# Performance work log

Hardware: AMD Instinct MI355X
Metric: run time of the kernel (lower is better)

## Reference

```python
import jax, jax.numpy as jnp
import numpy as np
import math

N = 8192
NFEAT = 63
NHID = 1024
NLAYERS = 7
LAMBDA = 1.5
ALPHA = 0.7
NEG = -1e12


def setup_inputs() -> dict:
    key = jax.random.key(0)
    ks = jax.random.split(key, 12)
    x = jax.random.normal(ks[0], (N, NFEAT), dtype=jnp.float32)
    # dist acts as a (normalized) propagation matrix; scale by 1/N for numerical stability
    dist = jax.random.uniform(ks[1], (N, N), dtype=jnp.float32) / N
    adj = jax.random.randint(ks[2], (N, N), 0, 2, dtype=jnp.int32)
    # parameters
    fc_W = jax.random.normal(ks[3], (NFEAT, NHID), dtype=jnp.float32) * 0.1
    fc_b = jnp.zeros((NHID,), dtype=jnp.float32)
    stdv = 1.0 / math.sqrt(NHID)
    conv_W = jax.random.uniform(ks[4], (NLAYERS, NHID, NHID), dtype=jnp.float32,
                                minval=-stdv, maxval=stdv)
    gat_W = jax.random.normal(ks[5], (NHID, NHID), dtype=jnp.float32) * (1.414 / math.sqrt(NHID))
    gat_a = jax.random.normal(ks[6], (2 * NHID, 1), dtype=jnp.float32) * 0.05
    cls1_W = jax.random.normal(ks[7], (NHID, 64), dtype=jnp.float32) * (1.0 / math.sqrt(NHID))
    cls1_b = jnp.zeros((64,), dtype=jnp.float32)
    cls3_W = jax.random.normal(ks[8], (64, 1), dtype=jnp.float32) * 0.125
    cls3_b = jnp.zeros((1,), dtype=jnp.float32)
    return {"x": x, "dist": dist, "adj": adj, "fc_W": fc_W, "fc_b": fc_b,
            "conv_W": conv_W, "gat_W": gat_W, "gat_a": gat_a,
            "cls1_W": cls1_W, "cls1_b": cls1_b, "cls3_W": cls3_W, "cls3_b": cls3_b}


def _theta(l):
    return min(1.0, math.log(LAMBDA / l + 1.0))


def reference(x, dist, adj, fc_W, fc_b, conv_W, gat_W, gat_a, cls1_W, cls1_b, cls3_W, cls3_b):
    # eval mode: all dropouts are identity
    h = jax.nn.relu(x @ fc_W + fc_b)          # [N, H]
    h0 = h
    # GCNII-style propagation layers
    for i in range(NLAYERS):
        theta = _theta(i + 1)
        hi = dist @ h                          # [N, H] sparse-style propagation
        support = (1.0 - ALPHA) * hi + ALPHA * h0
        out = theta * (support @ conv_W[i]) + (1.0 - theta) * support + h
        h = jax.nn.relu(out)
    # GAT layer (l = 9). Faithful math, but computed without the N*N*2F tensor:
    # e_ij = leakyrelu(h_i' @ a1 + h_j' @ a2) with h' = h @ W
    hp = h @ gat_W                             # [N, H]
    a1 = gat_a[:NHID, 0]                       # [H]
    a2 = gat_a[NHID:, 0]                       # [H]
    e = jax.nn.leaky_relu(hp @ a1[:, None] + (hp @ a2[:, None]).T, negative_slope=0.2)  # [N, N]
    e = jnp.where(adj > 0, e, NEG)
    attention = jax.nn.softmax(e, axis=1)      # [N, N]
    theta = _theta(9)
    hi = attention @ h                         # note: attends over layer input h, not hp
    support = (1.0 - ALPHA) * hi + ALPHA * h0
    out = theta * (support @ gat_W) + (1.0 - theta) * support + h
    h = jax.nn.elu(out)
    h = jax.nn.relu(h @ cls1_W + cls1_b)
    out = jax.nn.sigmoid(h @ cls3_W + cls3_b)  # [N, 1]
    return out.squeeze(-1)                     # [N]
```

## Files before the change

### kernel.cpp

```cpp
#include <hip/hip_runtime.h>
#include <math.h>

#define NN 8192
#define NH 1024

typedef __bf16 bf16x8 __attribute__((ext_vector_type(8)));
typedef float floatx4 __attribute__((ext_vector_type(4)));
typedef unsigned short us8 __attribute__((ext_vector_type(8)));
typedef unsigned short us;

__device__ __forceinline__ unsigned short f2bf(float f) {
  unsigned int u = __float_as_uint(f);
  u += 0x7fffu + ((u >> 16) & 1u);
  return (unsigned short)(u >> 16);
}

__device__ __forceinline__ void async16(const void* g, void* l) {
  __builtin_amdgcn_global_load_lds(
      (__attribute__((address_space(1))) void*)(g),
      (__attribute__((address_space(3))) void*)(l), 16, 0, 0);
}

__global__ __launch_bounds__(512)
void gemm_big(const us* __restrict__ A, const us* __restrict__ Bt,
              const float* __restrict__ aux, float* __restrict__ supf,
              us* __restrict__ supb)
{
  __shared__ __align__(16) us lsm[49152];
  us* lB = lsm;
  us* lA = lsm + 16384;

  const int id = blockIdx.x;
  const int yt = id & 31;
  const int xt = id >> 5;

  const int tid  = threadIdx.x;
  const int lane = tid & 63;
  const int wave = tid >> 6;
  const long tileM = (long)yt * 256;
  const long tileN = (long)xt * 128;
  const int wm = (wave & 3) * 64;
  const int wn = (wave >> 2) * 64;

  const int chunk = (tid & 3) ^ ((tid >> 3) & 3);
  const us* gAp = A + (tileM + (tid >> 2)) * 8192L + chunk * 8;
  const us* gBp = Bt + (tileN + (tid >> 2)) * 8192L + chunk * 8;
  const int lo = tid * 8;

  const int fr = lane & 15;
  const int q8 = (lane >> 4) * 8;
  const int q8x = q8 ^ ((fr & 6) << 2);

  floatx4 zero4 = {0.f, 0.f, 0.f, 0.f};
  floatx4 acc[4][4];
#pragma unroll
  for (int i = 0; i < 4; ++i)
#pragma unroll
    for (int j = 0; j < 4; ++j) acc[i][j] = zero4;

#define STAGE_BIG(s, kf)                                                  \
  {                                                                       \
    const long ko = (long)(kf) << 5;                                      \
    async16(gAp + ko, lA + (s)*8192 + lo);                                \
    async16(gAp + 128 * 8192L + ko, lA + (s)*8192 + 4096 + lo);           \
    async16(gBp + ko, lB + (s)*4096 + lo);                                \
  }

#define KSTEP_BIG(s, kf)                                                  \
  {                                                                       \
    asm volatile("s_waitcnt vmcnt(6)" ::: "memory");                      \
    __builtin_amdgcn_s_barrier();                                         \
    bf16x8 af[4], bfr[4];                                                 \
    _Pragma("unroll") for (int i = 0; i < 4; ++i)                         \
        af[i] = *(const bf16x8*)&lA[(s)*8192 + (wm + 16 * i + fr) * 32 + q8x]; \
    _Pragma("unroll") for (int j = 0; j < 4; ++j)                         \
        bfr[j] = *(const bf16x8*)&lB[(s)*4096 + (wn + 16 * j + fr) * 32 + q8x]; \
    STAGE_BIG((((s) + 3) & 3), kf);                                       \
    __builtin_amdgcn_s_barrier();                                         \
    asm volatile("s_waitcnt lgkmcnt(0)" ::: "memory");                    \
    __builtin_amdgcn_sched_barrier(0);                                    \
    __builtin_amdgcn_s_setprio(1);                                        \
    _Pragma("unroll") for (int i = 0; i < 4; ++i)                         \
        _Pragma("unroll") for (int j = 0; j < 4; ++j)                     \
            acc[i][j] = __builtin_amdgcn_mfma_f32_16x16x32_bf16(          \
                af[i], bfr[j], acc[i][j], 0, 0, 0);                       \
    __builtin_amdgcn_s_setprio(0);                                        \
    __builtin_amdgcn_sched_barrier(0);                                    \
  }

  STAGE_BIG(0, 0)
  STAGE_BIG(1, 1)
  STAGE_BIG(2, 2)

  for (int kt = 0; kt < 256; kt += 4) {
    int k3 = kt + 3; if (k3 > 255) k3 = 255;
    int k4 = kt + 4; if (k4 > 255) k4 = 255;
    int k5 = kt + 5; if (k5 > 255) k5 = 255;
    int k6 = kt + 6; if (k6 > 255) k6 = 255;
    KSTEP_BIG(0, k3)
    KSTEP_BIG(1, k4)
    KSTEP_BIG(2, k5)
    KSTEP_BIG(3, k6)
  }
  asm volatile("s_waitcnt vmcnt(0)" ::: "memory");

  const int crow = (lane >> 4) * 4;
#pragma unroll
  for (int i = 0; i < 4; ++i)
#pragma unroll
    for (int j = 0; j < 4; ++j)
#pragma unroll
      for (int r = 0; r < 4; ++r) {
        long row = tileM + wm + 16 * i + crow + r;
        long col = tileN + wn + 16 * j + fr;
        long idx = row * NH + col;
        float s = 0.3f * acc[i][j][r] + 0.7f * aux[idx];
        supf[idx] = s;
        supb[idx] = f2bf(s);
      }
#undef STAGE_BIG
#undef KSTEP_BIG
}

template<int EPI>
__global__ __launch_bounds__(256)
void gemm_db(const us* __restrict__ A, const us* __restrict__ Bt, int K,
             const float* __restrict__ aux, float* __restrict__ iof,
             us* __restrict__ outb, us* __restrict__ hTb, float theta)
{
  __shared__ __align__(16) us lsm[32768];
  us* lB = lsm;
  us* lA = lsm + 16384;

  const int id = blockIdx.x;
  const int xcd = id & 7, slot = id >> 3;
  const int xt = slot & 7;
  const int yt = xcd + 8 * (slot >> 3);

  const int tid  = threadIdx.x;
  const int lane = tid & 63;
  const int wave = tid >> 6;
  const long tileM = (long)yt * 128;
  const long tileN = (long)xt * 128;
  const int wm = (wave & 1) * 64;
  const int wn = (wave >> 1) * 64;

  const int chunk = (tid & 3) ^ ((tid >> 3) & 3);
  const us* gA0 = A + (tileM + (tid >> 2)) * (long)K + chunk * 8;
  const us* gA1 = gA0 + 64L * K;
  const us* gB0 = Bt + (tileN + (tid >> 2)) * (long)K + chunk * 8;
  const us* gB1 = gB0 + 64L * K;
  const int lo = tid * 8;

  const int fr = lane & 15;
  const int q8 = (lane >> 4) * 8;
  const int q8x = q8 ^ ((fr & 6) << 2);

  floatx4 zero4 = {0.f, 0.f, 0.f, 0.f};
  floatx4 acc[4][4];
#pragma unroll
  for (int i = 0; i < 4; ++i)
#pragma unroll
    for (int j = 0; j < 4; ++j) acc[i][j] = zero4;

#define STAGE_DB(s, kf)                                                   \
  {                                                                       \
    const int k0 = (kf) << 5;                                             \
    async16(gA0 + k0, lA + (s)*4096 + lo);                                \
    async16(gA1 + k0, lA + (s)*4096 + 2048 + lo);                         \
    async16(gB0 + k0, lB + (s)*4096 + lo);                                \
    async16(gB1 + k0, lB + (s)*4096 + 2048 + lo);                         \
  }

#define KSTEP_DB(s, kf)                                                   \
  {                                                                       \
    asm volatile("s_waitcnt vmcnt(8)" ::: "memory");                      \
    __builtin_amdgcn_s_barrier();                                         \
    bf16x8 af[4], bfr[4];                                                 \
    _Pragma("unroll") for (int i = 0; i < 4; ++i)                         \
        af[i] = *(const bf16x8*)&lA[(s)*4096 + (wm + 16 * i + fr) * 32 + q8x]; \
    _Pragma("unroll") for (int j = 0; j < 4; ++j)                         \
        bfr[j] = *(const bf16x8*)&lB[(s)*4096 + (wn + 16 * j + fr) * 32 + q8x]; \
    STAGE_DB((((s) + 3) & 3), kf);                                        \
    __builtin_amdgcn_s_barrier();                                         \
    asm volatile("s_waitcnt lgkmcnt(0)" ::: "memory");                    \
    __builtin_amdgcn_sched_barrier(0);                                    \
    __builtin_amdgcn_s_setprio(1);                                        \
    _Pragma("unroll") for (int i = 0; i < 4; ++i)                         \
        _Pragma("unroll") for (int j = 0; j < 4; ++j)                     \
            acc[i][j] = __builtin_amdgcn_mfma_f32_16x16x32_bf16(          \
                af[i], bfr[j], acc[i][j], 0, 0, 0);                       \
    __builtin_amdgcn_s_setprio(0);                                        \
    __builtin_amdgcn_sched_barrier(0);                                    \
  }

  STAGE_DB(0, 0)
  STAGE_DB(1, 1)
  STAGE_DB(2, 2)

  for (int kt = 0; kt < 32; kt += 4) {
    int k3 = kt + 3; if (k3 > 31) k3 = 31;
    int k4 = kt + 4; if (k4 > 31) k4 = 31;
    int k5 = kt + 5; if (k5 > 31) k5 = 31;
    int k6 = kt + 6; if (k6 > 31) k6 = 31;
    KSTEP_DB(0, k3)
    KSTEP_DB(1, k4)
    KSTEP_DB(2, k5)
    KSTEP_DB(3, k6)
  }
  asm volatile("s_waitcnt vmcnt(0)" ::: "memory");
  __syncthreads();

  us* ldsT = lsm;
  const int crow = (lane >> 4) * 4;
#pragma unroll
  for (int i = 0; i < 4; ++i) {
#pragma unroll
    for (int j = 0; j < 4; ++j) {
#pragma unroll
      for (int r = 0; r < 4; ++r) {
        int lr = wm + 16 * i + crow + r;
        int lc = wn + 16 * j + fr;
        long idx = (tileM + lr) * NH + tileN + lc;
        float o = theta * acc[i][j][r] + (1.f - theta) * aux[idx] + iof[idx];
        o = (EPI == 1) ? fmaxf(o, 0.f) : (o > 0.f ? o : __expf(o) - 1.f);
        iof[idx] = o;
        if (EPI == 1) ldsT[lc * 136 + lr] = f2bf(o);
        if (EPI == 2) outb[idx] = f2bf(o);
      }
    }
  }
  if (EPI == 1) {
    __syncthreads();
    int c = tid >> 1, half = tid & 1;
#pragma unroll
    for (int it = 0; it < 8; ++it) {
      int r = half * 64 + it * 8;
      us8 v = *(const us8*)&ldsT[c * 136 + r];
      *(us8*)&hTb[(tileN + c) * 8192L + tileM + r] = v;
    }
  }
#undef STAGE_DB
#undef KSTEP_DB
}

__global__ __launch_bounds__(256)
void cls_gemm(const us* __restrict__ hb, const us* __restrict__ W1t,
              const float* __restrict__ b1, const float* __restrict__ W3,
              const float* __restrict__ b3, float* __restrict__ out)
{
  __shared__ __align__(16) us lA[4096];
  __shared__ __align__(16) us lB[2048];
  const int tid = threadIdx.x, lane = tid & 63, wave = tid >> 6;
  const long tileM = (long)blockIdx.x * 128;
  const us* gA0 = hb + (tileM + (tid >> 2)) * 1024L + (tid & 3) * 8;
  const us* gA1 = gA0 + 64 * 1024L;
  const us* gB0 = W1t + (tid >> 2) * 1024L + (tid & 3) * 8;
  const int fr = lane & 15, q8 = (lane >> 4) * 8;
  const int wm = wave * 32;

  floatx4 zero4 = {0.f, 0.f, 0.f, 0.f};
  floatx4 acc[2][4];
#pragma unroll
  for (int i = 0; i < 2; ++i)
#pragma unroll
    for (int j = 0; j < 4; ++j) acc[i][j] = zero4;

  for (int kt = 0; kt < 32; ++kt) {
    const int k0 = kt << 5;
    async16(gA0 + k0, lA + tid * 8);
    async16(gA1 + k0, lA + 2048 + tid * 8);
    async16(gB0 + k0, lB + tid * 8);
    __syncthreads();
    bf16x8 af[2], bfr[4];
#pragma unroll
    for (int i = 0; i < 2; ++i)
      af[i] = *(const bf16x8*)&lA[(wm + 16 * i + fr) * 32 + q8];
#pragma unroll
    for (int j = 0; j < 4; ++j)
      bfr[j] = *(const bf16x8*)&lB[(16 * j + fr) * 32 + q8];
#pragma unroll
    for (int i = 0; i < 2; ++i)
#pragma unroll
      for (int j = 0; j < 4; ++j)
        acc[i][j] = __builtin_amdgcn_mfma_f32_16x16x32_bf16(af[i], bfr[j], acc[i][j], 0, 0, 0);
    __syncthreads();
  }

  float b1v[4], w3v[4];
#pragma unroll
  for (int j = 0; j < 4; ++j) { b1v[j] = b1[16 * j + fr]; w3v[j] = W3[16 * j + fr]; }
  const float b3v = b3[0];
  const int crow = (lane >> 4) * 4;
#pragma unroll
  for (int i = 0; i < 2; ++i)
#pragma unroll
    for (int r = 0; r < 4; ++r) {
      float v = 0.f;
#pragma unroll
      for (int j = 0; j < 4; ++j)
        v += fmaxf(acc[i][j][r] + b1v[j], 0.f) * w3v[j];
      v += __shfl_xor(v, 1);
      v += __shfl_xor(v, 2);
      v += __shfl_xor(v, 4);
      v += __shfl_xor(v, 8);
      if (fr == 0)
        out[tileM + wm + 16 * i + crow + r] = 1.f / (1.f + __expf(-(v + b3v)));
    }
}

__global__ __launch_bounds__(256)
void transpose_f32_bf16(const float* __restrict__ src, us* __restrict__ dst,
                        int R, int C) {
  __shared__ float t[32][33];
  int tid = threadIdx.x;
  int tx = tid & 31, ty = tid >> 5;
  long r0 = (long)blockIdx.y * 32, c0 = (long)blockIdx.x * 32;
#pragma unroll
  for (int i = 0; i < 32; i += 8)
    t[ty + i][tx] = src[(r0 + ty + i) * C + c0 + tx];
  __syncthreads();
#pragma unroll
  for (int i = 0; i < 32; i += 8)
    dst[(c0 + ty + i) * R + r0 + tx] = f2bf(t[tx][ty + i]);
}

__global__ __launch_bounds__(256)
void f32_to_bf16_vec(const float* __restrict__ s, us* __restrict__ d) {
  long i = (blockIdx.x * 256L + threadIdx.x) * 4;
  float4 v = *(const float4*)(s + i);
  *(ushort4*)(d + i) = make_ushort4(f2bf(v.x), f2bf(v.y), f2bf(v.z), f2bf(v.w));
}

__global__ __launch_bounds__(256)
void fc_kernel(const float* __restrict__ x, const float* __restrict__ W,
               const float* __restrict__ b, float* __restrict__ h0f,
               float* __restrict__ hf) {
  __shared__ float xs[64];
  int row = blockIdx.x, tid = threadIdx.x;
  if (tid < 63) xs[tid] = x[row * 63 + tid];
  __syncthreads();
#pragma unroll
  for (int q = 0; q < 4; ++q) {
    int c = tid + q * 256;
    float s = b[c];
    for (int k = 0; k < 63; ++k) s += xs[k] * W[k * NH + c];
    s = fmaxf(s, 0.f);
    long idx = (long)row * NH + c;
    h0f[idx] = s;
    hf[idx] = s;
  }
}

__global__ __launch_bounds__(256)
void wv_kernel(const float* __restrict__ W, const float* __restrict__ a,
               float* __restrict__ va1, float* __restrict__ va2) {
  int k = blockIdx.x, tid = threadIdx.x;
  float s1 = 0.f, s2 = 0.f;
  for (int n = tid; n < NH; n += 256) {
    float w = W[(long)k * NH + n];
    s1 += w * a[n];
    s2 += w * a[NH + n];
  }
#pragma unroll
  for (int o = 32; o; o >>= 1) { s1 += __shfl_down(s1, o); s2 += __shfl_down(s2, o); }
  __shared__ float r1[4], r2[4];
  int wave = tid >> 6;
  if ((tid & 63) == 0) { r1[wave] = s1; r2[wave] = s2; }
  __syncthreads();
  if (tid == 0) {
    va1[k] = r1[0] + r1[1] + r1[2] + r1[3];
    va2[k] = r2[0] + r2[1] + r2[2] + r2[3];
  }
}

__global__ __launch_bounds__(256)
void fg_kernel(const float* __restrict__ h, const float* __restrict__ va1,
               const float* __restrict__ va2, float* __restrict__ fv,
               float* __restrict__ gv) {
  int row = blockIdx.x, tid = threadIdx.x;
  float s1 = 0.f, s2 = 0.f;
  for (int k = tid; k < NH; k += 256) {
    float v = h[(long)row * NH + k];
    s1 += v * va1[k];
    s2 += v * va2[k];
  }
#pragma unroll
  for (int o = 32; o; o >>= 1) { s1 += __shfl_down(s1, o); s2 += __shfl_down(s2, o); }
  __shared__ float r1[4], r2[4];
  int wave = tid >> 6;
  if ((tid & 63) == 0) { r1[wave] = s1; r2[wave] = s2; }
  __syncthreads();
  if (tid == 0) {
    fv[row] = r1[0] + r1[1] + r1[2] + r1[3];
    gv[row] = r2[0] + r2[1] + r2[2] + r2[3];
  }
}

__global__ __launch_bounds__(256)
void attn_ml(const int* __restrict__ adj, const float* __restrict__ f,
             const float* __restrict__ g, float* __restrict__ Mr,
             float* __restrict__ Lr) {
  const int row = blockIdx.x, tid = threadIdx.x;
  const float fi = f[row];
  const int4* arow = (const int4*)(adj + (long)row * NN);
  float m = -3.0e38f, s = 0.f;
  for (int c = tid; c < NN / 4; c += 256) {
    int4 a = arow[c];
    float4 gg = *(const float4*)(g + c * 4);
#pragma unroll
    for (int t = 0; t < 4; ++t) {
      int av = (t == 0) ? a.x : (t == 1) ? a.y : (t == 2) ? a.z : a.w;
      float gvv = (t == 0) ? gg.x : (t == 1) ? gg.y : (t == 2) ? gg.z : gg.w;
      if (av > 0) {
        float e = fi + gvv;
        e = e > 0.f ? e : 0.2f * e;
        if (e > m) { s = s * __expf(m - e) + 1.f; m = e; }
        else s += __expf(e - m);
      }
    }
  }
#pragma unroll
  for (int o = 32; o; o >>= 1) {
    float m2 = __shfl_down(m, o), s2 = __shfl_down(s, o);
    float mn = fmaxf(m, m2);
    s = s * __expf(m - mn) + s2 * __expf(m2 - mn);
    m = mn;
  }
  __shared__ float ms[4], ss[4];
  int wave = tid >> 6;
  if ((tid & 63) == 0) { ms[wave] = m; ss[wave] = s; }
  __syncthreads();
  if (tid == 0) {
    float mm = ms[0], sv = ss[0];
    for (int w = 1; w < 4; ++w) {
      float mn = fmaxf(mm, ms[w]);
      sv = sv * __expf(mm - mn) + ss[w] * __expf(ms[w] - mn);
      mm = mn;
    }
    Mr[row] = mm;
    Lr[row] = sv;
  }
}

__global__ __launch_bounds__(256)
void attn_p(const int* __restrict__ adj, const float* __restrict__ f,
            const float* __restrict__ g, const float* __restrict__ Mr,
            const float* __restrict__ Lr, us* __restrict__ P) {
  long gid = blockIdx.x * 256L + threadIdx.x;
  int row = (int)(gid >> 11);
  int jc = (int)(gid & 2047) * 4;
  float fi = f[row], m = Mr[row], l = Lr[row];
  bool uni = !(l > 0.f);
  float inv = uni ? 0.f : 1.f / l;
  int4 a = *(const int4*)(adj + ((long)row << 13) + jc);
  float4 gg = *(const float4*)(g + jc);
  float p[4];
#pragma unroll
  for (int t = 0; t < 4; ++t) {
    int av = (t == 0) ? a.x : (t == 1) ? a.y : (t == 2) ? a.z : a.w;
    float gvv = (t == 0) ? gg.x : (t == 1) ? gg.y : (t == 2) ? gg.z : gg.w;
    float e = fi + gvv;
    e = e > 0.f ? e : 0.2f * e;
    float pv = (av > 0) ? __expf(e - m) * inv : 0.f;
    if (uni) pv = 1.f / (float)NN;
    p[t] = pv;
  }
  *(ushort4*)(P + ((long)row << 13) + jc) =
      make_ushort4(f2bf(p[0]), f2bf(p[1]), f2bf(p[2]), f2bf(p[3]));
}

extern "C" void kernel_launch(void* const* d_in, const int* in_sizes, int n_in,
                              void* d_out, int out_size, void* d_ws, size_t ws_size,
                              hipStream_t stream) {
  const float* x      = (const float*)d_in[0];
  const float* dist   = (const float*)d_in[1];
  const int*   adj    = (const int*)d_in[2];
  const float* fc_W   = (const float*)d_in[3];
  const float* fc_b   = (const float*)d_in[4];
  const float* conv_W = (const float*)d_in[5];
  const float* gat_W  = (const float*)d_in[6];
  const float* gat_a  = (const float*)d_in[7];
  const float* cls1_W = (const float*)d_in[8];
  const float* cls1_b = (const float*)d_in[9];
  const float* cls3_W = (const float*)d_in[10];
  const float* cls3_b = (const float*)d_in[11];
  float* out = (float*)d_out;

  char* p = (char*)d_ws;
  auto alloc = [&](size_t bytes) {
    char* r = p;
    p += (bytes + 255) & ~(size_t)255;
    return r;
  };
  us* distb   = (us*)alloc((size_t)NN * NN * 2);
  float* h0f  = (float*)alloc((size_t)NN * NH * 4);
  float* hf   = (float*)alloc((size_t)NN * NH * 4);
  float* supf = (float*)alloc((size_t)NN * NH * 4);
  us* supb    = (us*)alloc((size_t)NN * NH * 2);
  us* hb      = (us*)alloc((size_t)NN * NH * 2);
  us* hTb     = (us*)alloc((size_t)NN * NH * 2);
  us* convWT  = (us*)alloc((size_t)7 * NH * NH * 2);
  us* gatWT   = (us*)alloc((size_t)NH * NH * 2);
  us* W1t     = (us*)alloc((size_t)64 * NH * 2);
  float* va1 = (float*)alloc(NH * 4);
  float* va2 = (float*)alloc(NH * 4);
  float* fv  = (float*)alloc(NN * 4);
  float* gv  = (float*)alloc(NN * 4);
  float* Mr  = (float*)alloc(NN * 4);
  float* Lr  = (float*)alloc(NN * 4);

  float th[7];
  for (int l = 0; l < 7; ++l) {
    float t = logf(1.5f / (float)(l + 1) + 1.f);
    th[l] = t < 1.f ? t : 1.f;
  }
  float th9 = logf(1.5f / 9.f + 1.f);

  f32_to_bf16_vec<<<(NN * (long)NN) / (4 * 256), 256, 0, stream>>>(dist, distb);
  for (int i = 0; i < 7; ++i)
    transpose_f32_bf16<<<dim3(32, 32), 256, 0, stream>>>(
        conv_W + (size_t)i * NH * NH, convWT + (size_t)i * NH * NH, NH, NH);
  transpose_f32_bf16<<<dim3(32, 32), 256, 0, stream>>>(gat_W, gatWT, NH, NH);
  transpose_f32_bf16<<<dim3(2, 32), 256, 0, stream>>>(cls1_W, W1t, NH, 64);

  fc_kernel<<<NN, 256, 0, stream>>>(x, fc_W, fc_b, h0f, hf);
  transpose_f32_bf16<<<dim3(NH / 32, NN / 32), 256, 0, stream>>>(hf, hTb, NN, NH);

  for (int l = 0; l < 7; ++l) {
    gemm_big<<<256, 512, 0, stream>>>(distb, hTb, h0f, supf, supb);
    gemm_db<1><<<512, 256, 0, stream>>>(supb, convWT + (size_t)l * NH * NH, NH,
                                        supf, hf, nullptr, hTb, th[l]);
  }

  wv_kernel<<<NH, 256, 0, stream>>>(gat_W, gat_a, va1, va2);
  fg_kernel<<<NN, 256, 0, stream>>>(hf, va1, va2, fv, gv);
  attn_ml<<<NN, 256, 0, stream>>>(adj, fv, gv, Mr, Lr);
  attn_p<<<(NN * (long)NN) / (4 * 256), 256, 0, stream>>>(adj, fv, gv, Mr, Lr, distb);

  gemm_big<<<256, 512, 0, stream>>>(distb, hTb, h0f, supf, supb);
  gemm_db<2><<<512, 256, 0, stream>>>(supb, gatWT, NH, supf, hf, hb, nullptr, th9);

  cls_gemm<<<64, 256, 0, stream>>>(hb, W1t, cls1_b, cls3_W, cls3_b, out);
}
```

Before: 2.449 ms.

## Deepen big GEMM K-tile to 64 with 3-stage pipeline and single barrier

The large dist@h GEMM now loads K=64 slices per stage instead of 32, in a 3-stage LDS ring instead of 4, with an 8-way XOR swizzle matched to the wider rows. Each k-step issues the next stage's async loads right after one combined waitcnt+barrier and runs two MFMA sub-steps. This halves the number of barriers and loop iterations per unit of K. The smaller DB GEMM gets the same single-barrier reordering, with setprio and sched_barrier hints dropped in both kernels. The cost is larger LDS use (about 144 KB) and a launch-bounds hint for two blocks per CU, which LDS capacity probably cannot honour, plus shallower prefetch depth measured in stages.

```diff
diff --git a/kernel.cpp b/kernel.cpp
--- a/kernel.cpp
+++ b/kernel.cpp
@@ -21,14 +21,14 @@
       (__attribute__((address_space(3))) void*)(l), 16, 0, 0);
 }
 
-__global__ __launch_bounds__(512)
+__global__ __launch_bounds__(512, 2)
 void gemm_big(const us* __restrict__ A, const us* __restrict__ Bt,
               const float* __restrict__ aux, float* __restrict__ supf,
               us* __restrict__ supb)
 {
-  __shared__ __align__(16) us lsm[49152];
+  __shared__ __align__(16) us lsm[73728];
   us* lB = lsm;
-  us* lA = lsm + 16384;
+  us* lA = lsm + 24576;
 
   const int id = blockIdx.x;
   const int yt = id & 31;
@@ -42,14 +42,15 @@
   const int wm = (wave & 3) * 64;
   const int wn = (wave >> 2) * 64;
 
-  const int chunk = (tid & 3) ^ ((tid >> 3) & 3);
-  const us* gAp = A + (tileM + (tid >> 2)) * 8192L + chunk * 8;
-  const us* gBp = Bt + (tileN + (tid >> 2)) * 8192L + chunk * 8;
+  const int chunk8 = (tid & 7) ^ ((tid >> 3) & 7);
+  const us* gA0 = A + (tileM + (tid >> 3)) * 8192L + chunk8 * 8;
+  const us* gB0 = Bt + (tileN + (tid >> 3)) * 8192L + chunk8 * 8;
   const int lo = tid * 8;
 
   const int fr = lane & 15;
-  const int q8 = (lane >> 4) * 8;
-  const int q8x = q8 ^ ((fr & 6) << 2);
+  const int q  = lane >> 4;
+  const int cx0 = ((q) ^ (fr & 7)) * 8;
+  const int cx1 = ((4 + q) ^ (fr & 7)) * 8;
 
   floatx4 zero4 = {0.f, 0.f, 0.f, 0.f};
   floatx4 acc[4][4];
@@ -60,48 +61,45 @@
 
 #define STAGE_BIG(s, kf)                                                  \
   {                                                                       \
-    const long ko = (long)(kf) << 5;                                      \
-    async16(gAp + ko, lA + (s)*8192 + lo);                                \
-    async16(gAp + 128 * 8192L + ko, lA + (s)*8192 + 4096 + lo);           \
-    async16(gBp + ko, lB + (s)*4096 + lo);                                \
+    const long ko = (long)(kf) << 6;                                      \
+    async16(gA0 + ko,              lA + (s)*16384 + lo);                  \
+    async16(gA0 + 64 * 8192L + ko, lA + (s)*16384 + 4096 + lo);           \
+    async16(gA0 + 128 * 8192L + ko, lA + (s)*16384 + 8192 + lo);          \
+    async16(gA0 + 192 * 8192L + ko, lA + (s)*16384 + 12288 + lo);         \
+    async16(gB0 + ko,              lB + (s)*8192 + lo);                   \
+    async16(gB0 + 64 * 8192L + ko, lB + (s)*8192 + 4096 + lo);            \
   }
 
 #define KSTEP_BIG(s, kf)                                                  \
   {                                                                       \
-    asm volatile("s_waitcnt vmcnt(6)" ::: "memory");                      \
-    __builtin_amdgcn_s_barrier();                                         \
-    bf16x8 af[4], bfr[4];                                                 \
-    _Pragma("unroll") for (int i = 0; i < 4; ++i)                         \
-        af[i] = *(const bf16x8*)&lA[(s)*8192 + (wm + 16 * i + fr) * 32 + q8x]; \
-    _Pragma("unroll") for (int j = 0; j < 4; ++j)                         \
-        bfr[j] = *(const bf16x8*)&lB[(s)*4096 + (wn + 16 * j + fr) * 32 + q8x]; \
-    STAGE_BIG((((s) + 3) & 3), kf);                                       \
-    __builtin_amdgcn_s_barrier();                                         \
-    asm volatile("s_waitcnt lgkmcnt(0)" ::: "memory");                    \
-    __builtin_amdgcn_sched_barrier(0);                                    \
-    __builtin_amdgcn_s_setprio(1);                                        \
-    _Pragma("unroll") for (int i = 0; i < 4; ++i)                         \
+    asm volatile("s_waitcnt vmcnt(6)\n\ts_barrier" ::: "memory");         \
+    STAGE_BIG((((s) + 2) % 3), kf);                                       \
+    bf16x8 af[2][4], bfr[2][4];                                           \
+    _Pragma("unroll") for (int i = 0; i < 4; ++i) {                       \
+      af[0][i] = *(const bf16x8*)&lA[(s)*16384 + (wm + 16 * i + fr) * 64 + cx0]; \
+      af[1][i] = *(const bf16x8*)&lA[(s)*16384 + (wm + 16 * i + fr) * 64 + cx1]; \
+    }                                                                     \
+    _Pragma("unroll") for (int j = 0; j < 4; ++j) {                       \
+      bfr[0][j] = *(const bf16x8*)&lB[(s)*8192 + (wn + 16 * j + fr) * 64 + cx0]; \
+      bfr[1][j] = *(const bf16x8*)&lB[(s)*8192 + (wn + 16 * j + fr) * 64 + cx1]; \
+    }                                                                     \
+    _Pragma("unroll") for (int kk = 0; kk < 2; ++kk)                      \
+      _Pragma("unroll") for (int i = 0; i < 4; ++i)                       \
         _Pragma("unroll") for (int j = 0; j < 4; ++j)                     \
             acc[i][j] = __builtin_amdgcn_mfma_f32_16x16x32_bf16(          \
-                af[i], bfr[j], acc[i][j], 0, 0, 0);                       \
-    __builtin_amdgcn_s_setprio(0);                                        \
-    __builtin_amdgcn_sched_barrier(0);                                    \
+                af[kk][i], bfr[kk][j], acc[i][j], 0, 0, 0);               \
   }
 
   STAGE_BIG(0, 0)
   STAGE_BIG(1, 1)
-  STAGE_BIG(2, 2)
-
-  for (int kt = 0; kt < 256; kt += 4) {
-    int k3 = kt + 3; if (k3 > 255) k3 = 255;
-    int k4 = kt + 4; if (k4 > 255) k4 = 255;
-    int k5 = kt + 5; if (k5 > 255) k5 = 255;
-    int k6 = kt + 6; if (k6 > 255) k6 = 255;
-    KSTEP_BIG(0, k3)
-    KSTEP_BIG(1, k4)
-    KSTEP_BIG(2, k5)
-    KSTEP_BIG(3, k6)
-  }
+
+  for (int kt = 0; kt < 126; kt += 3) {
+    KSTEP_BIG(0, kt + 2)
+    KSTEP_BIG(1, kt + 3)
+    KSTEP_BIG(2, kt + 4)
+  }
+  KSTEP_BIG(0, 127)
+  KSTEP_BIG(1, 127)
   asm volatile("s_waitcnt vmcnt(0)" ::: "memory");
 
   const int crow = (lane >> 4) * 4;
@@ -174,24 +172,17 @@
 
 #define KSTEP_DB(s, kf)                                                   \
   {                                                                       \
-    asm volatile("s_waitcnt vmcnt(8)" ::: "memory");                      \
-    __builtin_amdgcn_s_barrier();                                         \
+    asm volatile("s_waitcnt vmcnt(8)\n\ts_barrier" ::: "memory");         \
+    STAGE_DB((((s) + 3) & 3), kf);                                        \
     bf16x8 af[4], bfr[4];                                                 \
     _Pragma("unroll") for (int i = 0; i < 4; ++i)                         \
         af[i] = *(const bf16x8*)&lA[(s)*4096 + (wm + 16 * i + fr) * 32 + q8x]; \
     _Pragma("unroll") for (int j = 0; j < 4; ++j)                         \
         bfr[j] = *(const bf16x8*)&lB[(s)*4096 + (wn + 16 * j + fr) * 32 + q8x]; \
-    STAGE_DB((((s) + 3) & 3), kf);                                        \
-    __builtin_amdgcn_s_barrier();                                         \
-    asm volatile("s_waitcnt lgkmcnt(0)" ::: "memory");                    \
-    __builtin_amdgcn_sched_barrier(0);                                    \
-    __builtin_amdgcn_s_setprio(1);                                        \
     _Pragma("unroll") for (int i = 0; i < 4; ++i)                         \
         _Pragma("unroll") for (int j = 0; j < 4; ++j)                     \
             acc[i][j] = __builtin_amdgcn_mfma_f32_16x16x32_bf16(          \
                 af[i], bfr[j], acc[i][j], 0, 0, 0);                       \
-    __builtin_amdgcn_s_setprio(0);                                        \
-    __builtin_amdgcn_sched_barrier(0);                                    \
   }
 
   STAGE_DB(0, 0)
```

Measured after the change: 2.190 ms. -10.5%, faster.
